# Kernel optimization log

Measured on AMD Instinct MI355X. Metric: run time of the kernel, lower is better.

The kernel has to match this reference:

```python
import jax, jax.numpy as jnp
import numpy as np

BATCH = 2048
TEMP = 0.5
EPS = 1e-12  # matches F.normalize default eps


def setup_inputs() -> dict:
    key = jax.random.key(0)
    k1, k2 = jax.random.split(key)
    emb_i = jax.random.normal(k1, (BATCH, 256), dtype=jnp.float32)
    emb_j = jax.random.normal(k2, (BATCH, 256), dtype=jnp.float32)
    return {"emb_i": emb_i, "emb_j": emb_j}


def _l2_normalize(x):
    norm = jnp.sqrt(jnp.sum(x * x, axis=1, keepdims=True))
    return x / jnp.maximum(norm, EPS)


def reference(emb_i, emb_j):
    n = emb_i.shape[0]  # = BATCH
    z_i = _l2_normalize(emb_i)
    z_j = _l2_normalize(emb_j)
    z = jnp.concatenate([z_i, z_j], axis=0)            # [2N, D]
    # cosine similarity of normalized vectors == plain GEMM
    sim = jnp.einsum('id,jd->ij', z, z)                # [2N, 2N]
    # positive pairs: diag offsets +N and -N
    sim_i_j = jnp.diagonal(sim, offset=n)              # [N]
    sim_j_i = jnp.diagonal(sim, offset=-n)             # [N]
    positives = jnp.concatenate([sim_i_j, sim_j_i])    # [2N]
    neg_mask = 1.0 - jnp.eye(2 * n, dtype=sim.dtype)   # [2N, 2N]
    numerator = jnp.exp(positives / TEMP)
    denominator = jnp.sum(neg_mask * jnp.exp(sim / TEMP), axis=1)  # [2N]
    loss_partial = -jnp.log(numerator / denominator)
    return jnp.sum(loss_partial) / (2 * n)
```

## Files before the change

kernel.cpp:

```cpp
#include <hip/hip_runtime.h>
#include <hip/hip_bf16.h>
#include <math.h>

#define NB        2048
#define TWO_N     4096
#define DIM       256
#define EPS       1e-12f
#define NT1D      (TWO_N / 128)
#define NTILES    (NT1D * (NT1D + 1) / 2)

typedef __attribute__((ext_vector_type(8))) short  bf16x8;
typedef __attribute__((ext_vector_type(4))) float  f32x4;

__global__ __launch_bounds__(256) void nrm_kernel(
    const float* __restrict__ emb_i, const float* __restrict__ emb_j,
    __hip_bfloat16* __restrict__ zb, float* __restrict__ pos,
    float* __restrict__ out)
{
    int t = threadIdx.x;
    int wave = t >> 6, lane = t & 63;
    int r = blockIdx.x * 4 + wave;
    float4 a = ((const float4*)(emb_i + (size_t)r * DIM))[lane];
    float4 b = ((const float4*)(emb_j + (size_t)r * DIM))[lane];
    float sa = a.x*a.x + a.y*a.y + a.z*a.z + a.w*a.w;
    float sb = b.x*b.x + b.y*b.y + b.z*b.z + b.w*b.w;
    float sd = a.x*b.x + a.y*b.y + a.z*b.z + a.w*b.w;
    #pragma unroll
    for (int off = 32; off >= 1; off >>= 1) {
        sa += __shfl_xor(sa, off, 64);
        sb += __shfl_xor(sb, off, 64);
        sd += __shfl_xor(sd, off, 64);
    }
    float si = 1.0f / fmaxf(sqrtf(sa), EPS);
    float sj = 1.0f / fmaxf(sqrtf(sb), EPS);

    union { __hip_bfloat16 h[4]; uint2 u; } pk;
    pk.h[0] = __float2bfloat16(a.x * si);
    pk.h[1] = __float2bfloat16(a.y * si);
    pk.h[2] = __float2bfloat16(a.z * si);
    pk.h[3] = __float2bfloat16(a.w * si);
    ((uint2*)(zb + (size_t)r * DIM))[lane] = pk.u;
    pk.h[0] = __float2bfloat16(b.x * sj);
    pk.h[1] = __float2bfloat16(b.y * sj);
    pk.h[2] = __float2bfloat16(b.z * sj);
    pk.h[3] = __float2bfloat16(b.w * sj);
    ((uint2*)(zb + (size_t)(r + NB) * DIM))[lane] = pk.u;

    if (lane == 0) pos[r] = sd * si * sj;
    if (blockIdx.x == 0 && t == 0) out[0] = 0.0f;
}

#define MFMA1(Av, Bv, m, n) \
    acc[m][n] = __builtin_amdgcn_mfma_f32_16x16x32_bf16(Av, Bv, acc[m][n], 0, 0, 0);

#define MFMA_ROW(Av, B0v, B1v, B2v, B3v, m) \
    MFMA1(Av, B0v, m, 0) MFMA1(Av, B1v, m, 1) \
    MFMA1(Av, B2v, m, 2) MFMA1(Av, B3v, m, 3)

#define MMSTEP(A0v, A1v, A2v, A3v, B0v, B1v, B2v, B3v) \
    MFMA_ROW(A0v, B0v, B1v, B2v, B3v, 0) \
    MFMA_ROW(A1v, B0v, B1v, B2v, B3v, 1) \
    MFMA_ROW(A2v, B0v, B1v, B2v, B3v, 2) \
    MFMA_ROW(A3v, B0v, B1v, B2v, B3v, 3)

#define LDSET(dA0, dA1, dA2, dA3, dB0, dB1, dB2, dB3, s) \
    dA0 = *(const bf16x8*)(apt0 + (s) * 32); \
    dA1 = *(const bf16x8*)(apt1 + (s) * 32); \
    dA2 = *(const bf16x8*)(apt2 + (s) * 32); \
    dA3 = *(const bf16x8*)(apt3 + (s) * 32); \
    dB0 = *(const bf16x8*)(bpt0 + (s) * 32); \
    dB1 = *(const bf16x8*)(bpt1 + (s) * 32); \
    dB2 = *(const bf16x8*)(bpt2 + (s) * 32); \
    dB3 = *(const bf16x8*)(bpt3 + (s) * 32);

#define SB __builtin_amdgcn_sched_barrier(0);

__global__ __launch_bounds__(256, 2) void simexp_kernel(
    const __hip_bfloat16* __restrict__ zb, float* __restrict__ part)
{
    int id = blockIdx.x;
    int by = (int)((sqrtf(8.0f * (float)id + 1.0f) - 1.0f) * 0.5f);
    while ((by + 1) * (by + 2) / 2 <= id) ++by;
    while (by * (by + 1) / 2 > id) --by;
    int bx = id - by * (by + 1) / 2;

    const short* Z = (const short*)zb;
    int t = threadIdx.x;
    int w = t >> 6, lane = t & 63;
    int quad = lane >> 4, c16 = lane & 15;
    int wm = w >> 1, wn = w & 1;
    int rbase = bx * 128 + wm * 64;
    int jbase = by * 128 + wn * 64;

    const short* apt0 = Z + (size_t)(rbase +  0 + c16) * DIM + quad * 8;
    const short* apt1 = Z + (size_t)(rbase + 16 + c16) * DIM + quad * 8;
    const short* apt2 = Z + (size_t)(rbase + 32 + c16) * DIM + quad * 8;
    const short* apt3 = Z + (size_t)(rbase + 48 + c16) * DIM + quad * 8;
    const short* bpt0 = Z + (size_t)(jbase +  0 + c16) * DIM + quad * 8;
    const short* bpt1 = Z + (size_t)(jbase + 16 + c16) * DIM + quad * 8;
    const short* bpt2 = Z + (size_t)(jbase + 32 + c16) * DIM + quad * 8;
    const short* bpt3 = Z + (size_t)(jbase + 48 + c16) * DIM + quad * 8;

    f32x4 acc[4][4];
    #pragma unroll
    for (int mt = 0; mt < 4; ++mt)
        #pragma unroll
        for (int nt = 0; nt < 4; ++nt)
            acc[mt][nt] = (f32x4){0.f, 0.f, 0.f, 0.f};

    bf16x8 A0, A1, A2, A3, B0, B1, B2, B3;
    bf16x8 P0, P1, P2, P3, Q0, Q1, Q2, Q3;
    bf16x8 R0, R1, R2, R3, S0, S1, S2, S3;
    bf16x8 U0, U1, U2, U3, V0, V1, V2, V3;

    LDSET(A0, A1, A2, A3, B0, B1, B2, B3, 0)
    LDSET(P0, P1, P2, P3, Q0, Q1, Q2, Q3, 1)
    LDSET(R0, R1, R2, R3, S0, S1, S2, S3, 2)
    LDSET(U0, U1, U2, U3, V0, V1, V2, V3, 3)
    SB
    MMSTEP(A0, A1, A2, A3, B0, B1, B2, B3)
    SB
    LDSET(A0, A1, A2, A3, B0, B1, B2, B3, 4)
    SB
    MMSTEP(P0, P1, P2, P3, Q0, Q1, Q2, Q3)
    SB
    LDSET(P0, P1, P2, P3, Q0, Q1, Q2, Q3, 5)
    SB
    MMSTEP(R0, R1, R2, R3, S0, S1, S2, S3)
    SB
    LDSET(R0, R1, R2, R3, S0, S1, S2, S3, 6)
    SB
    MMSTEP(U0, U1, U2, U3, V0, V1, V2, V3)
    SB
    LDSET(U0, U1, U2, U3, V0, V1, V2, V3, 7)
    SB
    MMSTEP(A0, A1, A2, A3, B0, B1, B2, B3)
    MMSTEP(P0, P1, P2, P3, Q0, Q1, Q2, Q3)
    MMSTEP(R0, R1, R2, R3, S0, S1, S2, S3)
    MMSTEP(U0, U1, U2, U3, V0, V1, V2, V3)

    float rsum[4][4];
    #pragma unroll
    for (int mt = 0; mt < 4; ++mt)
        #pragma unroll
        for (int rg = 0; rg < 4; ++rg) rsum[mt][rg] = 0.f;

    if (bx == by) {
        #pragma unroll
        for (int mt = 0; mt < 4; ++mt) {
            #pragma unroll
            for (int nt = 0; nt < 4; ++nt) {
                int j = jbase + nt * 16 + c16;
                #pragma unroll
                for (int rg = 0; rg < 4; ++rg) {
                    int r = rbase + mt * 16 + quad * 4 + rg;
                    float e = __expf(2.0f * acc[mt][nt][rg]);
                    rsum[mt][rg] += (r == j) ? 0.f : e;
                }
            }
        }
    } else {
        float csum[4] = {0.f, 0.f, 0.f, 0.f};
        #pragma unroll
        for (int mt = 0; mt < 4; ++mt) {
            #pragma unroll
            for (int nt = 0; nt < 4; ++nt) {
                #pragma unroll
                for (int rg = 0; rg < 4; ++rg) {
                    float e = __expf(2.0f * acc[mt][nt][rg]);
                    rsum[mt][rg] += e;
                    csum[nt] += e;
                }
            }
        }
        #pragma unroll
        for (int nt = 0; nt < 4; ++nt) {
            float v = csum[nt];
            v += __shfl_xor(v, 16, 64);
            v += __shfl_xor(v, 32, 64);
            if (quad == 0)
                part[(size_t)(by * 128 + wn * 64 + nt * 16 + c16) * 64
                     + 2 * bx + wm] = v;
        }
    }

    #pragma unroll
    for (int mt = 0; mt < 4; ++mt) {
        #pragma unroll
        for (int rg = 0; rg < 4; ++rg) {
            float v = rsum[mt][rg];
            v += __shfl_xor(v, 1, 64);
            v += __shfl_xor(v, 2, 64);
            v += __shfl_xor(v, 4, 64);
            v += __shfl_xor(v, 8, 64);
            if (c16 == 0)
                part[(size_t)(rbase + mt * 16 + quad * 4 + rg) * 64
                     + 2 * by + wn] = v;
        }
    }
}

__global__ __launch_bounds__(128) void redloss_kernel(
    const float* __restrict__ part, const float* __restrict__ pos,
    float* __restrict__ out)
{
    int s = blockIdx.x, t = threadIdx.x;
    int r = s * 128 + t;
    const float4* p = (const float4*)(part + ((size_t)r << 6));
    float sum = 0.f;
    #pragma unroll
    for (int i = 0; i < 16; ++i) {
        float4 v = p[i];
        sum += v.x + v.y + v.z + v.w;
    }
    float val = logf(sum) - 2.0f * pos[r & (NB - 1)];
    #pragma unroll
    for (int off = 32; off >= 1; off >>= 1) val += __shfl_xor(val, off, 64);
    __shared__ float red[2];
    if ((t & 63) == 0) red[t >> 6] = val;
    __syncthreads();
    if (t == 0)
        atomicAdd(out, (red[0] + red[1]) * (1.0f / (float)TWO_N));
}

extern "C" void kernel_launch(void* const* d_in, const int* in_sizes, int n_in,
                              void* d_out, int out_size, void* d_ws, size_t ws_size,
                              hipStream_t stream)
{
    const float* emb_i = (const float*)d_in[0];
    const float* emb_j = (const float*)d_in[1];
    float* out = (float*)d_out;

    __hip_bfloat16* zb = (__hip_bfloat16*)d_ws;
    float* part = (float*)((char*)d_ws + (size_t)TWO_N * DIM * sizeof(__hip_bfloat16));
    float* pos = part + (size_t)TWO_N * 64;

    nrm_kernel<<<NB / 4, 256, 0, stream>>>(emb_i, emb_j, zb, pos, out);
    simexp_kernel<<<NTILES, 256, 0, stream>>>(zb, part);
    redloss_kernel<<<NT1D, 128, 0, stream>>>(part, pos, out);
}
```

Measured before the change: 88.89 us.

## Store normalized embeddings in MFMA-fragment tiled layout for coalesced loads

The normalize kernel now writes the bf16 embeddings in a tiled layout, grouped into 16-row blocks with each 32-wide k-slice stored contiguously in MFMA fragment order. The similarity kernel can then fetch each fragment with one fully contiguous 1 KB wave load instead of strided row reads. This aims to improve coalescing and cache-line use in the global loads of the GEMM. In exchange the normalize kernel's stores become scattered 8-byte writes.

```diff
diff --git a/kernel.cpp b/kernel.cpp
--- a/kernel.cpp
+++ b/kernel.cpp
@@ -9,12 +9,13 @@
 #define NT1D      (TWO_N / 128)
 #define NTILES    (NT1D * (NT1D + 1) / 2)
 
+
 typedef __attribute__((ext_vector_type(8))) short  bf16x8;
 typedef __attribute__((ext_vector_type(4))) float  f32x4;
 
 __global__ __launch_bounds__(256) void nrm_kernel(
     const float* __restrict__ emb_i, const float* __restrict__ emb_j,
-    __hip_bfloat16* __restrict__ zb, float* __restrict__ pos,
+    short* __restrict__ zt, float* __restrict__ pos,
     float* __restrict__ out)
 {
     int t = threadIdx.x;
@@ -34,17 +35,20 @@
     float si = 1.0f / fmaxf(sqrtf(sa), EPS);
     float sj = 1.0f / fmaxf(sqrtf(sb), EPS);
 
+    int dst = (r >> 4) * 4096 + (lane >> 3) * 512 + ((lane >> 1) & 3) * 128
+            + (r & 15) * 8 + (lane & 1) * 4;
+
     union { __hip_bfloat16 h[4]; uint2 u; } pk;
     pk.h[0] = __float2bfloat16(a.x * si);
     pk.h[1] = __float2bfloat16(a.y * si);
     pk.h[2] = __float2bfloat16(a.z * si);
     pk.h[3] = __float2bfloat16(a.w * si);
-    ((uint2*)(zb + (size_t)r * DIM))[lane] = pk.u;
+    *(uint2*)(zt + dst) = pk.u;
     pk.h[0] = __float2bfloat16(b.x * sj);
     pk.h[1] = __float2bfloat16(b.y * sj);
     pk.h[2] = __float2bfloat16(b.z * sj);
     pk.h[3] = __float2bfloat16(b.w * sj);
-    ((uint2*)(zb + (size_t)(r + NB) * DIM))[lane] = pk.u;
+    *(uint2*)(zt + dst + 128 * 4096) = pk.u;
 
     if (lane == 0) pos[r] = sd * si * sj;
     if (blockIdx.x == 0 && t == 0) out[0] = 0.0f;
@@ -64,19 +68,19 @@
     MFMA_ROW(A3v, B0v, B1v, B2v, B3v, 3)
 
 #define LDSET(dA0, dA1, dA2, dA3, dB0, dB1, dB2, dB3, s) \
-    dA0 = *(const bf16x8*)(apt0 + (s) * 32); \
-    dA1 = *(const bf16x8*)(apt1 + (s) * 32); \
-    dA2 = *(const bf16x8*)(apt2 + (s) * 32); \
-    dA3 = *(const bf16x8*)(apt3 + (s) * 32); \
-    dB0 = *(const bf16x8*)(bpt0 + (s) * 32); \
-    dB1 = *(const bf16x8*)(bpt1 + (s) * 32); \
-    dB2 = *(const bf16x8*)(bpt2 + (s) * 32); \
-    dB3 = *(const bf16x8*)(bpt3 + (s) * 32);
+    dA0 = *(const bf16x8*)(apt0 + (s) * 512); \
+    dA1 = *(const bf16x8*)(apt1 + (s) * 512); \
+    dA2 = *(const bf16x8*)(apt2 + (s) * 512); \
+    dA3 = *(const bf16x8*)(apt3 + (s) * 512); \
+    dB0 = *(const bf16x8*)(bpt0 + (s) * 512); \
+    dB1 = *(const bf16x8*)(bpt1 + (s) * 512); \
+    dB2 = *(const bf16x8*)(bpt2 + (s) * 512); \
+    dB3 = *(const bf16x8*)(bpt3 + (s) * 512);
 
 #define SB __builtin_amdgcn_sched_barrier(0);
 
 __global__ __launch_bounds__(256, 2) void simexp_kernel(
-    const __hip_bfloat16* __restrict__ zb, float* __restrict__ part)
+    const short* __restrict__ zt, float* __restrict__ part)
 {
     int id = blockIdx.x;
     int by = (int)((sqrtf(8.0f * (float)id + 1.0f) - 1.0f) * 0.5f);
@@ -84,7 +88,7 @@
     while (by * (by + 1) / 2 > id) --by;
     int bx = id - by * (by + 1) / 2;
 
-    const short* Z = (const short*)zb;
+    const short* Z = zt;
     int t = threadIdx.x;
     int w = t >> 6, lane = t & 63;
     int quad = lane >> 4, c16 = lane & 15;
@@ -92,14 +96,14 @@
     int rbase = bx * 128 + wm * 64;
     int jbase = by * 128 + wn * 64;
 
-    const short* apt0 = Z + (size_t)(rbase +  0 + c16) * DIM + quad * 8;
-    const short* apt1 = Z + (size_t)(rbase + 16 + c16) * DIM + quad * 8;
-    const short* apt2 = Z + (size_t)(rbase + 32 + c16) * DIM + quad * 8;
-    const short* apt3 = Z + (size_t)(rbase + 48 + c16) * DIM + quad * 8;
-    const short* bpt0 = Z + (size_t)(jbase +  0 + c16) * DIM + quad * 8;
-    const short* bpt1 = Z + (size_t)(jbase + 16 + c16) * DIM + quad * 8;
-    const short* bpt2 = Z + (size_t)(jbase + 32 + c16) * DIM + quad * 8;
-    const short* bpt3 = Z + (size_t)(jbase + 48 + c16) * DIM + quad * 8;
+    const short* apt0 = Z + (size_t)((rbase >> 4) + 0) * 4096 + lane * 8;
+    const short* apt1 = Z + (size_t)((rbase >> 4) + 1) * 4096 + lane * 8;
+    const short* apt2 = Z + (size_t)((rbase >> 4) + 2) * 4096 + lane * 8;
+    const short* apt3 = Z + (size_t)((rbase >> 4) + 3) * 4096 + lane * 8;
+    const short* bpt0 = Z + (size_t)((jbase >> 4) + 0) * 4096 + lane * 8;
+    const short* bpt1 = Z + (size_t)((jbase >> 4) + 1) * 4096 + lane * 8;
+    const short* bpt2 = Z + (size_t)((jbase >> 4) + 2) * 4096 + lane * 8;
+    const short* bpt3 = Z + (size_t)((jbase >> 4) + 3) * 4096 + lane * 8;
 
     f32x4 acc[4][4];
     #pragma unroll
@@ -231,11 +235,11 @@
     const float* emb_j = (const float*)d_in[1];
     float* out = (float*)d_out;
 
-    __hip_bfloat16* zb = (__hip_bfloat16*)d_ws;
-    float* part = (float*)((char*)d_ws + (size_t)TWO_N * DIM * sizeof(__hip_bfloat16));
+    short* zt = (short*)d_ws;
+    float* part = (float*)((char*)d_ws + (size_t)TWO_N * DIM * sizeof(short));
     float* pos = part + (size_t)TWO_N * 64;
 
-    nrm_kernel<<<NB / 4, 256, 0, stream>>>(emb_i, emb_j, zb, pos, out);
-    simexp_kernel<<<NTILES, 256, 0, stream>>>(zb, part);
+    nrm_kernel<<<NB / 4, 256, 0, stream>>>(emb_i, emb_j, zt, pos, out);
+    simexp_kernel<<<NTILES, 256, 0, stream>>>(zt, part);
     redloss_kernel<<<NT1D, 128, 0, stream>>>(part, pos, out);
 }
```

New measurement: 77.39 us. 1.15x faster.
